# Performance work log

Measured on AMD Instinct MI355X. Metric: run time of the kernel, lower is better.

## Reference

```python
import jax, jax.numpy as jnp
import numpy as np

N, E = 50000, 800000
IN_CH, OUT_CH, HEADS = 128, 64, 4
NEG_SLOPE = 0.2
BN_EPS = 1e-5


def setup_inputs() -> dict:
    key = jax.random.key(0)
    ks = jax.random.split(key, 8)
    x = jax.random.normal(ks[0], (N, IN_CH), dtype=jnp.float32)
    edge_index = jax.random.randint(ks[1], (2, E), 0, N, dtype=jnp.int64)
    # GATConv params (concat=False: W projects to H*C, output averaged over heads)
    W = jax.random.normal(ks[2], (IN_CH, HEADS * OUT_CH), dtype=jnp.float32) * (1.0 / np.sqrt(IN_CH))
    att_src = jax.random.normal(ks[3], (HEADS, OUT_CH), dtype=jnp.float32) * 0.1
    att_dst = jax.random.normal(ks[4], (HEADS, OUT_CH), dtype=jnp.float32) * 0.1
    bias = jnp.zeros((OUT_CH,), dtype=jnp.float32)
    bn_weight = jnp.ones((OUT_CH,), dtype=jnp.float32)
    bn_bias = jnp.zeros((OUT_CH,), dtype=jnp.float32)
    return {"x": x, "edge_index": edge_index, "W": W, "att_src": att_src,
            "att_dst": att_dst, "bias": bias, "bn_weight": bn_weight, "bn_bias": bn_bias}


def reference(x, edge_index, W, att_src, att_dst, bias, bn_weight, bn_bias):
    # dropout p=0.3 on input and attention weights: identity in eval mode
    n = x.shape[0]
    x_proj = (x @ W).reshape(n, HEADS, OUT_CH)              # [N, H, C]
    a_src = jnp.einsum('nhc,hc->nh', x_proj, att_src)       # [N, H]
    a_dst = jnp.einsum('nhc,hc->nh', x_proj, att_dst)       # [N, H]

    # PyG default add_self_loops=True
    loops = jnp.arange(n, dtype=edge_index.dtype)
    src = jnp.concatenate([edge_index[0], loops])           # [E+N]
    dst = jnp.concatenate([edge_index[1], loops])           # [E+N]

    e = jax.nn.leaky_relu(a_src[src] + a_dst[dst], NEG_SLOPE)  # [E+N, H]
    # edge-softmax per destination node (numerically stable)
    m = jax.ops.segment_max(e, dst, num_segments=n)         # [N, H]
    ex = jnp.exp(e - m[dst])
    denom = jax.ops.segment_sum(ex, dst, num_segments=n)    # [N, H]
    alpha = ex / denom[dst]                                 # [E+N, H]

    msg = alpha[:, :, None] * x_proj[src]                   # [E+N, H, C]
    out = jax.ops.segment_sum(msg, dst, num_segments=n)     # [N, H, C]
    out = out.mean(axis=1) + bias                           # concat=False -> head mean

    # BatchNorm (training-mode batch statistics, biased variance)
    mu = out.mean(axis=0)
    var = out.var(axis=0)
    out = (out - mu) * jax.lax.rsqrt(var + BN_EPS) * bn_weight + bn_bias
    return jax.nn.elu(out)
```

## Files before the change

kernel.cpp:

```cpp
#include <hip/hip_runtime.h>

#define IN_CH 128
#define HC 256
#define OUT_CH 64
#define NEG 0.2f
#define BN_EPS 1e-5f
#define APITCH 136
#define CSR_CAP 4096

typedef __attribute__((ext_vector_type(8))) short short8v;
typedef __attribute__((ext_vector_type(4))) float f32x4v;

__device__ __forceinline__ float4 add4(float4 a, float4 b) {
    return make_float4(a.x + b.x, a.y + b.y, a.z + b.z, a.w + b.w);
}
__device__ __forceinline__ float4 mul4(float4 a, float4 b) {
    return make_float4(a.x * b.x, a.y * b.y, a.z * b.z, a.w * b.w);
}
__device__ __forceinline__ float4 exp4f(float4 a) {
    return make_float4(__expf(a.x), __expf(a.y), __expf(a.z), __expf(a.w));
}
__device__ __forceinline__ float4 leaky4(float4 v) {
    v.x = v.x > 0.f ? v.x : v.x * NEG;
    v.y = v.y > 0.f ? v.y : v.y * NEG;
    v.z = v.z > 0.f ? v.z : v.z * NEG;
    v.w = v.w > 0.f ? v.w : v.w * NEG;
    return v;
}
__device__ __forceinline__ unsigned short f2bf(float f) {
    unsigned u = __float_as_uint(f);
    unsigned r = u + 0x7fffu + ((u >> 16) & 1u);
    return (unsigned short)(r >> 16);
}
__device__ __forceinline__ void acc8(float4& a, float ws, unsigned u) {
    a.x += ws * (float)(u & 0xffu);
    a.y += ws * (float)((u >> 8) & 0xffu);
    a.z += ws * (float)((u >> 16) & 0xffu);
    a.w += ws * (float)(u >> 24);
}

__global__ __launch_bounds__(256) void prep_wt(const float* __restrict__ W,
                                               unsigned short* __restrict__ wt,
                                               unsigned* __restrict__ zeros, int nz) {
    int idx = blockIdx.x * 256 + threadIdx.x;
    if (idx < nz) zeros[idx] = 0u;
    if (idx >= 64 * 64) return;
    int frag = idx >> 6, l = idx & 63;
    int j = frag >> 2, ks = frag & 3;
    int c = l & 15, g = l >> 4;
    int ch = c * 16 + j;
    int k0 = ks * 32 + g * 8;
    unsigned up[4];
    #pragma unroll
    for (int q = 0; q < 4; ++q) {
        unsigned short lo = f2bf(W[(size_t)(k0 + 2 * q) * HC + ch]);
        unsigned short hi = f2bf(W[(size_t)(k0 + 2 * q + 1) * HC + ch]);
        up[q] = (unsigned)lo | ((unsigned)hi << 16);
    }
    *(uint4*)(wt + (size_t)idx * 8) = make_uint4(up[0], up[1], up[2], up[3]);
}

__global__ __launch_bounds__(256) void gemm_and_scatter(const float* __restrict__ x,
                                                        const unsigned short* __restrict__ wt,
                                                        const float* __restrict__ att_src,
                                                        const float* __restrict__ att_dst,
                                                        unsigned char* __restrict__ xq,
                                                        float* __restrict__ pks,
                                                        float* __restrict__ adst, int N,
                                                        const int* __restrict__ ei,
                                                        unsigned* __restrict__ bucket_cnt,
                                                        unsigned* __restrict__ bucketbuf,
                                                        int E, int gemmBlocks) {
    __shared__ unsigned short Al[64][APITCH];
    __shared__ unsigned lcnt[512], lbase[512], lcur[512];
    int t = threadIdx.x;

    if ((int)blockIdx.x >= gemmBlocks) {
        lcnt[t] = 0u; lcnt[t + 256] = 0u;
        lcur[t] = 0u; lcur[t + 256] = 0u;
        __syncthreads();
        int c0 = ((int)blockIdx.x - gemmBlocks) * 4096;
        unsigned rec[16];
        int bk[16];
        #pragma unroll
        for (int i = 0; i < 16; ++i) {
            int e = c0 + t + i * 256;
            bk[i] = -1;
            if (e < E) {
                unsigned s = (unsigned)ei[e];
                unsigned d = (unsigned)ei[E + e];
                rec[i] = s | ((d & 127u) << 16);
                bk[i] = (int)(d >> 7);
                atomicAdd(&lcnt[bk[i]], 1u);
            }
        }
        __syncthreads();
        #pragma unroll
        for (int h = 0; h < 2; ++h) {
            int bi = t + h * 256;
            lbase[bi] = lcnt[bi] ? atomicAdd(&bucket_cnt[bi], lcnt[bi]) : 0u;
        }
        __syncthreads();
        #pragma unroll
        for (int i = 0; i < 16; ++i) {
            if (bk[i] >= 0) {
                unsigned p = lbase[bk[i]] + atomicAdd(&lcur[bk[i]], 1u);
                if (p < CSR_CAP) bucketbuf[(size_t)bk[i] * CSR_CAP + p] = rec[i];
            }
        }
        return;
    }

    int r0 = blockIdx.x * 64;
    #pragma unroll
    for (int i = 0; i < 8; ++i) {
        int f4 = t + i * 256;
        int m = f4 >> 5, kf = f4 & 31;
        float4 v = make_float4(0.f, 0.f, 0.f, 0.f);
        int r = r0 + m;
        if (r < N) v = *(const float4*)(x + (size_t)r * IN_CH + kf * 4);
        ushort4 pk;
        pk.x = f2bf(v.x); pk.y = f2bf(v.y); pk.z = f2bf(v.z); pk.w = f2bf(v.w);
        *(ushort4*)(&Al[m][kf * 4]) = pk;
    }
    __syncthreads();

    int w = t >> 6, l = t & 63;
    int c = l & 15, g = l >> 4;
    int arow = w * 16 + c;

    f32x4v acc[16];
    #pragma unroll
    for (int j = 0; j < 16; ++j) acc[j] = (f32x4v){0.f, 0.f, 0.f, 0.f};

    #pragma unroll
    for (int ks = 0; ks < 4; ++ks) {
        short8v a = *(const short8v*)(&Al[arow][ks * 32 + g * 8]);
        #pragma unroll
        for (int j = 0; j < 16; ++j) {
            short8v b = *(const short8v*)(wt + (size_t)((j * 4 + ks) * 64 + l) * 8);
            acc[j] = __builtin_amdgcn_mfma_f32_16x16x32_bf16(a, b, acc[j], 0, 0, 0);
        }
    }

    float as_c[16], ad_c[16];
    #pragma unroll
    for (int q = 0; q < 4; ++q) {
        *(float4*)(&as_c[q * 4]) = *(const float4*)(att_src + c * 16 + q * 4);
        *(float4*)(&ad_c[q * 4]) = *(const float4*)(att_dst + c * 16 + q * 4);
    }
    #pragma unroll
    for (int i = 0; i < 4; ++i) {
        int r = r0 + w * 16 + g * 4 + i;
        float ps = 0.f, pd = 0.f;
        float amax = 0.f;
        #pragma unroll
        for (int j = 0; j < 16; ++j) {
            float av = acc[j][i];
            ps += av * as_c[j];
            pd += av * ad_c[j];
            amax = fmaxf(amax, fabsf(av));
        }
        ps += __shfl_xor(ps, 1, 64); pd += __shfl_xor(pd, 1, 64);
        ps += __shfl_xor(ps, 2, 64); pd += __shfl_xor(pd, 2, 64);
        amax = fmaxf(amax, __shfl_xor(amax, 1, 64));
        amax = fmaxf(amax, __shfl_xor(amax, 2, 64));
        float inv = amax > 0.f ? 127.f / amax : 0.f;
        if (r < N) {
            int q4 = c & 3, h = c >> 2;
            if (q4 == 0) pks[(size_t)r * 8 + h] = ps;
            else if (q4 == 1) adst[(size_t)r * 4 + h] = pd;
            else if (q4 == 2) pks[(size_t)r * 8 + 4 + h] = amax * (1.f / 127.f);
            unsigned* orow = (unsigned*)(xq + (size_t)r * HC);
            #pragma unroll
            for (int q = 0; q < 4; ++q) {
                unsigned b0 = (unsigned)(int)fmaf(acc[q * 4 + 0][i], inv, 128.5f);
                unsigned b1 = (unsigned)(int)fmaf(acc[q * 4 + 1][i], inv, 128.5f);
                unsigned b2 = (unsigned)(int)fmaf(acc[q * 4 + 2][i], inv, 128.5f);
                unsigned b3 = (unsigned)(int)fmaf(acc[q * 4 + 3][i], inv, 128.5f);
                unsigned pk = b0 | (b1 << 8) | (b2 << 16) | (b3 << 24);
                orow[(((c & 3) * 4 + q) << 2) + h] = pk;
            }
        }
    }
}

__global__ __launch_bounds__(512) void bucket_csr(const unsigned* __restrict__ bucketbuf,
                                                  const unsigned* __restrict__ bucket_cnt,
                                                  unsigned* __restrict__ rowptr,
                                                  unsigned short* __restrict__ ssrc,
                                                  int N, int E, int NB) {
    __shared__ unsigned csum[512];
    __shared__ unsigned dcnt[128], dscan[128], curo[128];
    __shared__ unsigned short sstage[CSR_CAP];
    int b = blockIdx.x, t = threadIdx.x;
    csum[t] = (t < NB) ? bucket_cnt[t] : 0u;
    if (t < 128) dcnt[t] = 0u;
    __syncthreads();
    for (int o = 1; o < 512; o <<= 1) {
        unsigned v = (t >= o) ? csum[t - o] : 0u;
        __syncthreads();
        csum[t] += v;
        __syncthreads();
    }
    unsigned base = (b == 0) ? 0u : csum[b - 1];
    unsigned nloc = bucket_cnt[b];
    if (nloc > CSR_CAP) nloc = CSR_CAP;
    const unsigned* bb = bucketbuf + (size_t)b * CSR_CAP;
    for (unsigned i = t; i < nloc; i += 512) atomicAdd(&dcnt[bb[i] >> 16], 1u);
    __syncthreads();
    if (t < 128) dscan[t] = dcnt[t];
    __syncthreads();
    for (int o = 1; o < 128; o <<= 1) {
        unsigned v = 0u;
        if (t < 128 && t >= o) v = dscan[t - o];
        __syncthreads();
        if (t < 128) dscan[t] += v;
        __syncthreads();
    }
    if (t < 128) {
        unsigned loff = dscan[t] - dcnt[t];
        curo[t] = loff;
        int node = b * 128 + t;
        if (node < N) rowptr[node] = base + loff;
    }
    if (b == 0 && t == 0) rowptr[N] = (unsigned)E;
    __syncthreads();
    for (unsigned i = t; i < nloc; i += 512) {
        unsigned r = bb[i];
        unsigned p = atomicAdd(&curo[r >> 16], 1u);
        sstage[p] = (unsigned short)(r & 0xffffu);
    }
    __syncthreads();
    for (unsigned i = t; i < nloc; i += 512) ssrc[base + i] = sstage[i];
}

__global__ __launch_bounds__(256) void node_fused(const unsigned short* __restrict__ ssrc,
                                                  const unsigned* __restrict__ rowptr,
                                                  const float* __restrict__ pks,
                                                  const float* __restrict__ adst,
                                                  const unsigned char* __restrict__ xq,
                                                  float* __restrict__ out, int N) {
    int wid = (blockIdx.x * 256 + threadIdx.x) >> 5;
    if (wid >= N) return;
    int hlane = threadIdx.x & 31;
    int row0 = rowptr[wid];
    int deg = (int)rowptr[wid + 1] - row0;

    float4 ad = *(const float4*)(adst + (size_t)wid * 4);
    float4 saw = *(const float4*)(pks + (size_t)wid * 8);
    float4 scw = *(const float4*)(pks + (size_t)wid * 8 + 4);

    bool isEdge = hlane < deg;
    bool active = hlane <= deg;
    int s0 = wid;
    float4 as_s = saw, sc_s = scw;
    if (isEdge) {
        s0 = ssrc[row0 + hlane];
        as_s = *(const float4*)(pks + (size_t)s0 * 8);
        sc_s = *(const float4*)(pks + (size_t)s0 * 8 + 4);
    }
    float4 ex0 = make_float4(0.f, 0.f, 0.f, 0.f);
    if (deg < 32 ? active : true) ex0 = exp4f(leaky4(add4(as_s, ad)));
    float4 sum = ex0;
    if (deg >= 32) {
        for (int j = hlane + 32; j < deg; j += 32) {
            int s = ssrc[row0 + j];
            float4 lv = leaky4(add4(*(const float4*)(pks + (size_t)s * 8), ad));
            sum = add4(sum, exp4f(lv));
        }
        if (hlane == 31) sum = add4(sum, exp4f(leaky4(add4(saw, ad))));
    }
    #pragma unroll
    for (int m = 1; m < 32; m <<= 1) {
        sum.x += __shfl_xor(sum.x, m, 32);
        sum.y += __shfl_xor(sum.y, m, 32);
        sum.z += __shfl_xor(sum.z, m, 32);
        sum.w += __shfl_xor(sum.w, m, 32);
    }
    float4 inv4 = make_float4(0.25f / sum.x, 0.25f / sum.y, 0.25f / sum.z, 0.25f / sum.w);
    float4 wsv = mul4(mul4(ex0, sc_s), inv4);

    int grp = hlane >> 4, sub = hlane & 15;
    float4 acc = make_float4(0.f, 0.f, 0.f, 0.f);
    float wssum = 0.f;

    if (deg < 32) {
        int nIter = (deg + 2) >> 1;
        #pragma unroll 4
        for (int it = 0; it < nIter; ++it) {
            int e = it * 2 + grp;
            int ec = e < 32 ? e : 0;
            int s = __shfl(s0, ec, 32);
            float w0 = __shfl(wsv.x, ec, 32), w1 = __shfl(wsv.y, ec, 32);
            float w2 = __shfl(wsv.z, ec, 32), w3 = __shfl(wsv.w, ec, 32);
            if (e >= 32) { w0 = w1 = w2 = w3 = 0.f; s = wid; }
            uint4 u = *(const uint4*)(xq + (size_t)s * HC + sub * 16);
            acc8(acc, w0, u.x); acc8(acc, w1, u.y);
            acc8(acc, w2, u.z); acc8(acc, w3, u.w);
            wssum += w0 + w1 + w2 + w3;
        }
    } else {
        float4 selfws = mul4(mul4(exp4f(leaky4(add4(saw, ad))), scw), inv4);
        for (int jb = 0; jb <= deg; jb += 2) {
            int e = jb + grp;
            int ec = e < 32 ? e : 0;
            int s_sh = __shfl(s0, ec, 32);
            float w0 = __shfl(wsv.x, ec, 32), w1 = __shfl(wsv.y, ec, 32);
            float w2 = __shfl(wsv.z, ec, 32), w3 = __shfl(wsv.w, ec, 32);
            int s;
            float4 wv4;
            if (e < deg) {
                if (e < 32) {
                    s = s_sh;
                    wv4 = make_float4(w0, w1, w2, w3);
                } else {
                    s = ssrc[row0 + e];
                    float4 glv = leaky4(add4(*(const float4*)(pks + (size_t)s * 8), ad));
                    float4 gsc = *(const float4*)(pks + (size_t)s * 8 + 4);
                    wv4 = mul4(mul4(exp4f(glv), gsc), inv4);
                }
            } else if (e == deg) {
                s = wid; wv4 = selfws;
            } else {
                s = wid; wv4 = make_float4(0.f, 0.f, 0.f, 0.f);
            }
            uint4 u = *(const uint4*)(xq + (size_t)s * HC + sub * 16);
            acc8(acc, wv4.x, u.x); acc8(acc, wv4.y, u.y);
            acc8(acc, wv4.z, u.z); acc8(acc, wv4.w, u.w);
            wssum += wv4.x + wv4.y + wv4.z + wv4.w;
        }
    }

    acc.x += __shfl_xor(acc.x, 16, 32);
    acc.y += __shfl_xor(acc.y, 16, 32);
    acc.z += __shfl_xor(acc.z, 16, 32);
    acc.w += __shfl_xor(acc.w, 16, 32);
    wssum += __shfl_xor(wssum, 16, 32);
    float off = 128.f * wssum;
    if (hlane < 16) {
        float4 o4 = make_float4(acc.x - off, acc.y - off, acc.z - off, acc.w - off);
        *(float4*)(out + (size_t)wid * OUT_CH + sub * 4) = o4;
    }
}

__global__ __launch_bounds__(256) void bn_stats(const float* __restrict__ out,
                                                float* __restrict__ sums,
                                                float* __restrict__ sqs, int N) {
    int c = threadIdx.x & 63, rl = threadIdx.x >> 6;
    float s = 0.f, q = 0.f;
    for (int r = blockIdx.x * 4 + rl; r < N; r += gridDim.x * 4) {
        float v = out[(size_t)r * 64 + c];
        s += v; q += v * v;
    }
    __shared__ float sb[256], qb[256];
    sb[threadIdx.x] = s; qb[threadIdx.x] = q;
    __syncthreads();
    if (rl == 0) {
        s = sb[c] + sb[64 + c] + sb[128 + c] + sb[192 + c];
        q = qb[c] + qb[64 + c] + qb[128 + c] + qb[192 + c];
        atomicAdd(sums + c, s);
        atomicAdd(sqs + c, q);
    }
}

__global__ __launch_bounds__(256) void finalize(float* __restrict__ out,
                                                const float* __restrict__ bnw,
                                                const float* __restrict__ bnb,
                                                const float* __restrict__ sums,
                                                const float* __restrict__ sqs, int N) {
    int idx = blockIdx.x * 256 + threadIdx.x;
    if (idx >= N * 64) return;
    int c = idx & 63;
    float invN = 1.0f / (float)N;
    float mu = sums[c] * invN;
    float var = sqs[c] * invN - mu * mu;
    float v = out[idx];
    float y = (v - mu) * rsqrtf(var + BN_EPS) * bnw[c] + bnb[c];
    out[idx] = y > 0.f ? y : expm1f(y);
}

extern "C" void kernel_launch(void* const* d_in, const int* in_sizes, int n_in,
                              void* d_out, int out_size, void* d_ws, size_t ws_size,
                              hipStream_t stream) {
    const float* x       = (const float*)d_in[0];
    const int*   ei      = (const int*)d_in[1];
    const float* W       = (const float*)d_in[2];
    const float* att_src = (const float*)d_in[3];
    const float* att_dst = (const float*)d_in[4];
    const float* bnw     = (const float*)d_in[6];
    const float* bnb     = (const float*)d_in[7];
    int N = in_sizes[0] / IN_CH;
    int E = in_sizes[1] / 2;
    float* out = (float*)d_out;
    int NB = (N + 127) / 128;

    unsigned char*  xq        = (unsigned char*)d_ws;
    unsigned short* wt        = (unsigned short*)(xq + (size_t)N * HC);
    float*          pks       = (float*)(wt + 64 * 64 * 8);
    float*          adst      = pks + (size_t)N * 8;
    unsigned*       bucket_cnt= (unsigned*)(adst + (size_t)N * 4);
    float*          sums      = (float*)(bucket_cnt + 512);
    float*          sqs       = sums + 64;
    unsigned*       rowptr    = (unsigned*)(sqs + 64);
    unsigned*       bucketbuf = rowptr + N + 1;
    unsigned short* ssrc      = (unsigned short*)(bucketbuf + (size_t)NB * CSR_CAP);

    prep_wt<<<16, 256, 0, stream>>>(W, wt, bucket_cnt, 640);

    int gemmBlocks = (N + 63) / 64;
    int scatBlocks = (E + 4095) / 4096;
    gemm_and_scatter<<<gemmBlocks + scatBlocks, 256, 0, stream>>>(
        x, wt, att_src, att_dst, xq, pks, adst, N, ei, bucket_cnt, bucketbuf, E, gemmBlocks);

    bucket_csr<<<NB, 512, 0, stream>>>(bucketbuf, bucket_cnt, rowptr, ssrc, N, E, NB);

    int gn = (N + 7) / 8;
    node_fused<<<gn, 256, 0, stream>>>(ssrc, rowptr, pks, adst, xq, out, N);

    bn_stats<<<1024, 256, 0, stream>>>(out, sums, sqs, N);
    finalize<<<((N * 64) + 255) / 256, 256, 0, stream>>>(out, bnw, bnb, sums, sqs, N);
}
```

Baseline: 119.3 us.

## Move edge-softmax weight computation into CSR build kernel

The bucket_csr kernel now computes the per-edge attention exponentials, accumulates per-destination denominators in shared-memory atomics, and writes normalized per-edge weights, self-loop weights and weight sums to global buffers. node_fused then only streams the precomputed weights and the quantized features, dropping its warp-level softmax reduction and the special path for degree 32 and above. The aim is to remove the second pass over pks and the shuffles in the aggregation kernel. In exchange it adds a float4-per-edge global write and read, larger shared-memory use in bucket_csr that may lower its occupancy, and fp16 rounding of the intermediate exp times scale values.

Measured after the change: 162.0 us. +35.7%, slower.

```diff
diff --git a/kernel.cpp b/kernel.cpp
--- a/kernel.cpp
+++ b/kernel.cpp
@@ -1,4 +1,5 @@
 #include <hip/hip_runtime.h>
+#include <hip/hip_fp16.h>
 
 #define IN_CH 128
 #define HC 256
@@ -31,6 +32,16 @@
     unsigned u = __float_as_uint(f);
     unsigned r = u + 0x7fffu + ((u >> 16) & 1u);
     return (unsigned short)(r >> 16);
+}
+__device__ __forceinline__ unsigned pkh2(float a, float b) {
+    return (unsigned)__half_as_ushort(__float2half_rn(a)) |
+           ((unsigned)__half_as_ushort(__float2half_rn(b)) << 16);
+}
+__device__ __forceinline__ float h2lo(unsigned u) {
+    return __half2float(__ushort_as_half((unsigned short)(u & 0xffffu)));
+}
+__device__ __forceinline__ float h2hi(unsigned u) {
+    return __half2float(__ushort_as_half((unsigned short)(u >> 16)));
 }
 __device__ __forceinline__ void acc8(float4& a, float ws, unsigned u) {
     a.x += ws * (float)(u & 0xffu);
@@ -187,15 +198,35 @@
 
 __global__ __launch_bounds__(512) void bucket_csr(const unsigned* __restrict__ bucketbuf,
                                                   const unsigned* __restrict__ bucket_cnt,
+                                                  const float* __restrict__ pks,
+                                                  const float* __restrict__ adst,
                                                   unsigned* __restrict__ rowptr,
                                                   unsigned short* __restrict__ ssrc,
+                                                  float* __restrict__ wsbuf,
+                                                  float* __restrict__ selfws,
+                                                  float* __restrict__ wssumbuf,
                                                   int N, int E, int NB) {
     __shared__ unsigned csum[512];
     __shared__ unsigned dcnt[128], dscan[128], curo[128];
-    __shared__ unsigned short sstage[CSR_CAP];
+    __shared__ unsigned sstage[CSR_CAP];
+    __shared__ uint2 exws[CSR_CAP];
+    __shared__ float4 dadst[128], dsaw[128], dscw[128], dden[128];
+    __shared__ float dwssum[128];
     int b = blockIdx.x, t = threadIdx.x;
     csum[t] = (t < NB) ? bucket_cnt[t] : 0u;
-    if (t < 128) dcnt[t] = 0u;
+    if (t < 128) {
+        dcnt[t] = 0u;
+        int node = b * 128 + t;
+        if (node < N) {
+            dadst[t] = *(const float4*)(adst + (size_t)node * 4);
+            dsaw[t]  = *(const float4*)(pks + (size_t)node * 8);
+            dscw[t]  = *(const float4*)(pks + (size_t)node * 8 + 4);
+        } else {
+            dadst[t] = make_float4(0.f, 0.f, 0.f, 0.f);
+            dsaw[t] = dadst[t]; dscw[t] = dadst[t];
+        }
+        dden[t] = make_float4(0.f, 0.f, 0.f, 0.f);
+    }
     __syncthreads();
     for (int o = 1; o < 512; o <<= 1) {
         unsigned v = (t >= o) ? csum[t - o] : 0u;
@@ -229,16 +260,55 @@
     for (unsigned i = t; i < nloc; i += 512) {
         unsigned r = bb[i];
         unsigned p = atomicAdd(&curo[r >> 16], 1u);
-        sstage[p] = (unsigned short)(r & 0xffffu);
-    }
-    __syncthreads();
-    for (unsigned i = t; i < nloc; i += 512) ssrc[base + i] = sstage[i];
+        sstage[p] = r;
+    }
+    __syncthreads();
+    for (unsigned i = t; i < nloc; i += 512) {
+        unsigned r = sstage[i];
+        int s = (int)(r & 0xffffu), d = (int)(r >> 16);
+        float4 as4 = *(const float4*)(pks + (size_t)s * 8);
+        float4 sc4 = *(const float4*)(pks + (size_t)s * 8 + 4);
+        float4 ex = exp4f(leaky4(add4(as4, dadst[d])));
+        exws[i] = make_uint2(pkh2(ex.x * sc4.x, ex.y * sc4.y),
+                             pkh2(ex.z * sc4.z, ex.w * sc4.w));
+        float* dd = (float*)&dden[d];
+        atomicAdd(dd + 0, ex.x); atomicAdd(dd + 1, ex.y);
+        atomicAdd(dd + 2, ex.z); atomicAdd(dd + 3, ex.w);
+    }
+    __syncthreads();
+    if (t < 128) {
+        int node = b * 128 + t;
+        float4 selfex = exp4f(leaky4(add4(dsaw[t], dadst[t])));
+        float4 den = add4(dden[t], selfex);
+        float4 inv = make_float4(0.25f / den.x, 0.25f / den.y, 0.25f / den.z, 0.25f / den.w);
+        dden[t] = inv;
+        float4 sws = mul4(mul4(selfex, dscw[t]), inv);
+        if (node < N) *(float4*)(selfws + (size_t)node * 4) = sws;
+        dwssum[t] = sws.x + sws.y + sws.z + sws.w;
+    }
+    __syncthreads();
+    for (unsigned i = t; i < nloc; i += 512) {
+        unsigned r = sstage[i];
+        int s = (int)(r & 0xffffu), d = (int)(r >> 16);
+        uint2 e2 = exws[i];
+        float4 exs = make_float4(h2lo(e2.x), h2hi(e2.x), h2lo(e2.y), h2hi(e2.y));
+        float4 ws = mul4(exs, dden[d]);
+        *(float4*)(wsbuf + (size_t)(base + i) * 4) = ws;
+        atomicAdd(&dwssum[d], ws.x + ws.y + ws.z + ws.w);
+        ssrc[base + i] = (unsigned short)s;
+    }
+    __syncthreads();
+    if (t < 128) {
+        int node = b * 128 + t;
+        if (node < N) wssumbuf[node] = dwssum[t];
+    }
 }
 
 __global__ __launch_bounds__(256) void node_fused(const unsigned short* __restrict__ ssrc,
                                                   const unsigned* __restrict__ rowptr,
-                                                  const float* __restrict__ pks,
-                                                  const float* __restrict__ adst,
+                                                  const float* __restrict__ wsbuf,
+                                                  const float* __restrict__ selfws,
+                                                  const float* __restrict__ wssumbuf,
                                                   const unsigned char* __restrict__ xq,
                                                   float* __restrict__ out, int N) {
     int wid = (blockIdx.x * 256 + threadIdx.x) >> 5;
@@ -246,98 +316,35 @@
     int hlane = threadIdx.x & 31;
     int row0 = rowptr[wid];
     int deg = (int)rowptr[wid + 1] - row0;
-
-    float4 ad = *(const float4*)(adst + (size_t)wid * 4);
-    float4 saw = *(const float4*)(pks + (size_t)wid * 8);
-    float4 scw = *(const float4*)(pks + (size_t)wid * 8 + 4);
-
-    bool isEdge = hlane < deg;
-    bool active = hlane <= deg;
-    int s0 = wid;
-    float4 as_s = saw, sc_s = scw;
-    if (isEdge) {
-        s0 = ssrc[row0 + hlane];
-        as_s = *(const float4*)(pks + (size_t)s0 * 8);
-        sc_s = *(const float4*)(pks + (size_t)s0 * 8 + 4);
-    }
-    float4 ex0 = make_float4(0.f, 0.f, 0.f, 0.f);
-    if (deg < 32 ? active : true) ex0 = exp4f(leaky4(add4(as_s, ad)));
-    float4 sum = ex0;
-    if (deg >= 32) {
-        for (int j = hlane + 32; j < deg; j += 32) {
-            int s = ssrc[row0 + j];
-            float4 lv = leaky4(add4(*(const float4*)(pks + (size_t)s * 8), ad));
-            sum = add4(sum, exp4f(lv));
-        }
-        if (hlane == 31) sum = add4(sum, exp4f(leaky4(add4(saw, ad))));
-    }
-    #pragma unroll
-    for (int m = 1; m < 32; m <<= 1) {
-        sum.x += __shfl_xor(sum.x, m, 32);
-        sum.y += __shfl_xor(sum.y, m, 32);
-        sum.z += __shfl_xor(sum.z, m, 32);
-        sum.w += __shfl_xor(sum.w, m, 32);
-    }
-    float4 inv4 = make_float4(0.25f / sum.x, 0.25f / sum.y, 0.25f / sum.z, 0.25f / sum.w);
-    float4 wsv = mul4(mul4(ex0, sc_s), inv4);
-
     int grp = hlane >> 4, sub = hlane & 15;
+
     float4 acc = make_float4(0.f, 0.f, 0.f, 0.f);
-    float wssum = 0.f;
-
-    if (deg < 32) {
-        int nIter = (deg + 2) >> 1;
-        #pragma unroll 4
-        for (int it = 0; it < nIter; ++it) {
-            int e = it * 2 + grp;
-            int ec = e < 32 ? e : 0;
-            int s = __shfl(s0, ec, 32);
-            float w0 = __shfl(wsv.x, ec, 32), w1 = __shfl(wsv.y, ec, 32);
-            float w2 = __shfl(wsv.z, ec, 32), w3 = __shfl(wsv.w, ec, 32);
-            if (e >= 32) { w0 = w1 = w2 = w3 = 0.f; s = wid; }
-            uint4 u = *(const uint4*)(xq + (size_t)s * HC + sub * 16);
-            acc8(acc, w0, u.x); acc8(acc, w1, u.y);
-            acc8(acc, w2, u.z); acc8(acc, w3, u.w);
-            wssum += w0 + w1 + w2 + w3;
-        }
-    } else {
-        float4 selfws = mul4(mul4(exp4f(leaky4(add4(saw, ad))), scw), inv4);
-        for (int jb = 0; jb <= deg; jb += 2) {
-            int e = jb + grp;
-            int ec = e < 32 ? e : 0;
-            int s_sh = __shfl(s0, ec, 32);
-            float w0 = __shfl(wsv.x, ec, 32), w1 = __shfl(wsv.y, ec, 32);
-            float w2 = __shfl(wsv.z, ec, 32), w3 = __shfl(wsv.w, ec, 32);
-            int s;
-            float4 wv4;
-            if (e < deg) {
-                if (e < 32) {
-                    s = s_sh;
-                    wv4 = make_float4(w0, w1, w2, w3);
-                } else {
-                    s = ssrc[row0 + e];
-                    float4 glv = leaky4(add4(*(const float4*)(pks + (size_t)s * 8), ad));
-                    float4 gsc = *(const float4*)(pks + (size_t)s * 8 + 4);
-                    wv4 = mul4(mul4(exp4f(glv), gsc), inv4);
-                }
-            } else if (e == deg) {
-                s = wid; wv4 = selfws;
-            } else {
-                s = wid; wv4 = make_float4(0.f, 0.f, 0.f, 0.f);
-            }
-            uint4 u = *(const uint4*)(xq + (size_t)s * HC + sub * 16);
-            acc8(acc, wv4.x, u.x); acc8(acc, wv4.y, u.y);
-            acc8(acc, wv4.z, u.z); acc8(acc, wv4.w, u.w);
-            wssum += wv4.x + wv4.y + wv4.z + wv4.w;
-        }
+    int nIter = (deg + 2) >> 1;
+    #pragma unroll 4
+    for (int it = 0; it < nIter; ++it) {
+        int e = it * 2 + grp;
+        int s;
+        float4 ws4;
+        if (e < deg) {
+            s = ssrc[row0 + e];
+            ws4 = *(const float4*)(wsbuf + (size_t)(row0 + e) * 4);
+        } else if (e == deg) {
+            s = wid;
+            ws4 = *(const float4*)(selfws + (size_t)wid * 4);
+        } else {
+            s = wid;
+            ws4 = make_float4(0.f, 0.f, 0.f, 0.f);
+        }
+        uint4 u = *(const uint4*)(xq + (size_t)s * HC + sub * 16);
+        acc8(acc, ws4.x, u.x); acc8(acc, ws4.y, u.y);
+        acc8(acc, ws4.z, u.z); acc8(acc, ws4.w, u.w);
     }
 
     acc.x += __shfl_xor(acc.x, 16, 32);
     acc.y += __shfl_xor(acc.y, 16, 32);
     acc.z += __shfl_xor(acc.z, 16, 32);
     acc.w += __shfl_xor(acc.w, 16, 32);
-    wssum += __shfl_xor(wssum, 16, 32);
-    float off = 128.f * wssum;
+    float off = 128.f * wssumbuf[wid];
     if (hlane < 16) {
         float4 o4 = make_float4(acc.x - off, acc.y - off, acc.z - off, acc.w - off);
         *(float4*)(out + (size_t)wid * OUT_CH + sub * 4) = o4;
@@ -404,7 +411,10 @@
     float*          sqs       = sums + 64;
     unsigned*       rowptr    = (unsigned*)(sqs + 64);
     unsigned*       bucketbuf = rowptr + N + 1;
-    unsigned short* ssrc      = (unsigned short*)(bucketbuf + (size_t)NB * CSR_CAP);
+    float*          wsbuf     = (float*)(bucketbuf + (size_t)NB * CSR_CAP);
+    float*          selfws    = wsbuf + (size_t)E * 4;
+    float*          wssumbuf  = selfws + (size_t)N * 4;
+    unsigned short* ssrc      = (unsigned short*)(wssumbuf + N);
 
     prep_wt<<<16, 256, 0, stream>>>(W, wt, bucket_cnt, 640);
 
@@ -413,10 +423,11 @@
     gemm_and_scatter<<<gemmBlocks + scatBlocks, 256, 0, stream>>>(
         x, wt, att_src, att_dst, xq, pks, adst, N, ei, bucket_cnt, bucketbuf, E, gemmBlocks);
 
-    bucket_csr<<<NB, 512, 0, stream>>>(bucketbuf, bucket_cnt, rowptr, ssrc, N, E, NB);
+    bucket_csr<<<NB, 512, 0, stream>>>(bucketbuf, bucket_cnt, pks, adst,
+                                       rowptr, ssrc, wsbuf, selfws, wssumbuf, N, E, NB);
 
     int gn = (N + 7) / 8;
-    node_fused<<<gn, 256, 0, stream>>>(ssrc, rowptr, pks, adst, xq, out, N);
+    node_fused<<<gn, 256, 0, stream>>>(ssrc, rowptr, wsbuf, selfws, wssumbuf, xq, out, N);
 
     bn_stats<<<1024, 256, 0, stream>>>(out, sums, sqs, N);
     finalize<<<((N * 64) + 255) / 256, 256, 0, stream>>>(out, bnw, bnb, sums, sqs, N);
```
